# Performance work log

Measured on AMD Instinct MI355X. Metric: run time of the kernel, lower is better.

Reference implementation:

```python
import jax, jax.numpy as jnp
import numpy as np

D = 128      # input_dim (= out_channels = edge_dim)
H = 2        # n_head
N_ENT = 100000
B = 64       # number of queries / batches
R = 500      # number of relations
E = 400000   # number of original edges
NEG = 0.2    # GATv2 leaky_relu negative slope


def setup_inputs() -> dict:
    key = jax.random.key(0)
    ks = jax.random.split(key, 10)
    s = 1.0 / np.sqrt(D)
    queries = jax.random.normal(ks[0], (B, D), jnp.float32)
    entities = jax.random.normal(ks[1], (N_ENT, D), jnp.float32)
    edge_index = jax.random.randint(ks[2], (2, E), 0, N_ENT)
    relations = jax.random.normal(ks[3], (R, D), jnp.float32)
    relation_index = jax.random.randint(ks[4], (E,), 0, R)
    # guarantees batch.max()+1 == queries.shape[0] (module assert)
    batch = jnp.arange(N_ENT, dtype=jnp.int32) % B
    # GATv2Conv params: lin_l / lin_r (bias=True), lin_edge (bias=False), att, bias
    W_l = jax.random.normal(ks[5], (H * D, D), jnp.float32) * s
    b_l = jnp.zeros((H * D,), jnp.float32)
    W_r = jax.random.normal(ks[6], (H * D, D), jnp.float32) * s
    b_r = jnp.zeros((H * D,), jnp.float32)
    W_ea = jax.random.normal(ks[7], (H * D, D), jnp.float32) * s
    att = jax.random.normal(ks[8], (H, D), jnp.float32) * s
    bias = jnp.zeros((D,), jnp.float32)  # concat=False -> size out_channels
    # outer Injector.lin_edge: Linear(H*D, D, bias=True)
    W_le = jax.random.normal(ks[9], (D, H * D), jnp.float32) / np.sqrt(H * D)
    b_le = jnp.zeros((D,), jnp.float32)
    return dict(queries=queries, entities=entities, edge_index=edge_index,
                relations=relations, relation_index=relation_index, batch=batch,
                W_l=W_l, b_l=b_l, W_r=W_r, b_r=b_r, W_ea=W_ea, att=att,
                bias=bias, W_le=W_le, b_le=b_le)


def reference(queries, entities, edge_index, relations, relation_index, batch,
              W_l, b_l, W_r, b_r, W_ea, att, bias, W_le, b_le):
    n_ent = entities.shape[0]
    node = jnp.vstack([entities, queries])                        # [N+B, D]
    rel_feat = jnp.vstack([relations,
                           jnp.ones((1, relations.shape[1]), relations.dtype)])
    # added edges: query -> its entities
    src = jnp.concatenate([edge_index[0], batch.astype(edge_index.dtype) + n_ent])
    tgt = jnp.concatenate([edge_index[1],
                           jnp.arange(n_ent, dtype=edge_index.dtype)])
    rel_idx = jnp.concatenate([relation_index,
                               jnp.full((n_ent,), rel_feat.shape[0] - 1,
                                        relation_index.dtype)])
    edge_attr = rel_feat[rel_idx]                                  # [Etot, D]

    n_tot = node.shape[0]
    x_l = (node @ W_l.T + b_l).reshape(n_tot, H, D)                # source proj
    x_r = (node @ W_r.T + b_r).reshape(n_tot, H, D)                # target proj
    e = (edge_attr @ W_ea.T).reshape(-1, H, D)                     # [Etot, H, D]

    xj = x_l[src]                                                  # gather per edge
    z = jax.nn.leaky_relu(xj + x_r[tgt] + e, NEG)                  # [Etot, H, D]
    alpha = jnp.einsum('ehd,hd->eh', z, att)                       # [Etot, H]
    # segment softmax over target nodes
    amax = jax.ops.segment_max(alpha, tgt, num_segments=n_tot)
    alpha = jnp.exp(alpha - amax[tgt])
    denom = jax.ops.segment_sum(alpha, tgt, num_segments=n_tot)
    alpha = alpha / (denom[tgt] + 1e-16)

    msg = xj * alpha[..., None]                                    # [Etot, H, D]
    agg = jax.ops.segment_sum(msg, tgt, num_segments=n_tot)        # [Ntot, H, D]
    out = agg.mean(axis=1) + bias                                  # concat=False
    out_node = out[:n_ent]

    out_edge = jax.nn.relu(relations @ W_ea.T)                     # [R, H*D]
    out_edge = out_edge @ W_le.T + b_le                            # [R, D]
    return (out_node, out_edge)
```

## Files before the change

### kernel.cpp

```cpp
#include <hip/hip_runtime.h>
#include <math.h>

#define D 128
#define HD 256
#define N_ENT 100000
#define NBATCH 64
#define NTOT (N_ENT + NBATCH)
#define RCOUNT 500
#define E_BASE 400000
#define ETOT (E_BASE + N_ENT)
#define NEG 0.2f
#define SCAN_NB 391
#define CPAD (SCAN_NB * 256)

#define WCAST_NB 64
#define ZERO_NB SCAN_NB
#define REL_NB (RCOUNT + 1)
#define PREP_NB (WCAST_NB + ZERO_NB + REL_NB)

#define GEMM_NB ((NTOT + 63) / 64)
#define HIST_NB ((ETOT + 255) / 256)
#define EDGE_TPW 8
#define EDGE_NB (N_ENT / (4 * EDGE_TPW))

typedef __attribute__((ext_vector_type(8))) short bf16x8;
typedef __attribute__((ext_vector_type(8))) unsigned short u16x8;
typedef __attribute__((ext_vector_type(4))) float f32x4;
typedef __attribute__((ext_vector_type(2))) float f32x2;

static __device__ __forceinline__ unsigned cvt_pk_bf16(float lo, float hi) {
  unsigned r;
  asm("v_cvt_pk_bf16_f32 %0, %1, %2" : "=v"(r) : "v"(lo), "v"(hi));
  return r;
}
static __device__ __forceinline__ unsigned short f2bf_hw(float f) {
  unsigned r;
  asm("v_cvt_pk_bf16_f32 %0, %1, %1" : "=v"(r) : "v"(f));
  return (unsigned short)r;
}
static __device__ __forceinline__ f32x2 bfpair(unsigned u) {
  f32x2 r;
  r[0] = __builtin_bit_cast(float, u << 16);
  r[1] = __builtin_bit_cast(float, u & 0xffff0000u);
  return r;
}

static __device__ __forceinline__ float dpp_red16(float p) {
  int t;
  t = __builtin_amdgcn_update_dpp(0, __builtin_bit_cast(int, p), 0xB1, 0xF, 0xF, true);
  p += __builtin_bit_cast(float, t);
  t = __builtin_amdgcn_update_dpp(0, __builtin_bit_cast(int, p), 0x4E, 0xF, 0xF, true);
  p += __builtin_bit_cast(float, t);
  t = __builtin_amdgcn_update_dpp(0, __builtin_bit_cast(int, p), 0x141, 0xF, 0xF, true);
  p += __builtin_bit_cast(float, t);
  t = __builtin_amdgcn_update_dpp(0, __builtin_bit_cast(int, p), 0x140, 0xF, 0xF, true);
  p += __builtin_bit_cast(float, t);
  return p;
}

__global__ __launch_bounds__(256) void k_prep(
    const float* __restrict__ W_l, const float* __restrict__ W_r,
    unsigned short* __restrict__ Wbf,
    const float* __restrict__ relations, const float* __restrict__ W_ea,
    const float* __restrict__ W_le, const float* __restrict__ b_le,
    unsigned short* __restrict__ e_rel, float* __restrict__ out_edge,
    int* __restrict__ counts) {
  __shared__ float relu_p[HD];
  int bx = blockIdx.x;
  int tid = threadIdx.x;
  if (bx < WCAST_NB) {
    int e4 = (bx * 256 + tid) * 4;
    int v = e4 >> 7;
    int k = e4 & 127;
    const float* src = (v < HD) ? (W_l + (size_t)v * D + k) : (W_r + (size_t)(v - HD) * D + k);
    float4 a = *(const float4*)src;
    uint2 p;
    p.x = cvt_pk_bf16(a.x, a.y);
    p.y = cvt_pk_bf16(a.z, a.w);
    *(uint2*)(Wbf + (size_t)v * D + k) = p;
    return;
  }
  if (bx < WCAST_NB + ZERO_NB) {
    counts[(bx - WCAST_NB) * 256 + tid] = 0;
    return;
  }
  int r = bx - (WCAST_NB + ZERO_NB);
  int j = tid;
  const float* w = W_ea + (size_t)j * D;
  float acc = 0.f;
  if (r < RCOUNT) {
    const float* rel = relations + (size_t)r * D;
    for (int k = 0; k < D; k += 4) {
      float4 a = *(const float4*)(rel + k);
      float4 b = *(const float4*)(w + k);
      acc += a.x * b.x + a.y * b.y + a.z * b.z + a.w * b.w;
    }
  } else {
    for (int k = 0; k < D; k += 4) {
      float4 b = *(const float4*)(w + k);
      acc += b.x + b.y + b.z + b.w;
    }
  }
  e_rel[(size_t)r * HD + j] = f2bf_hw(acc);
  if (r < RCOUNT) {
    relu_p[j] = acc > 0.f ? acc : 0.f;
    __syncthreads();
    if (j < D) {
      const float* wl = W_le + (size_t)j * HD;
      float o = b_le[j];
      for (int k = 0; k < HD; k += 4) {
        float4 p4 = *(const float4*)(relu_p + k);
        float4 w4 = *(const float4*)(wl + k);
        o += p4.x * w4.x + p4.y * w4.y + p4.z * w4.z + p4.w * w4.w;
      }
      out_edge[(size_t)r * D + j] = o;
    }
  }
}

#define LDA 136

__global__ __launch_bounds__(256) void k_gemm_mfma(
    const float* __restrict__ entities, const float* __restrict__ queries,
    const unsigned short* __restrict__ Wbf,
    const float* __restrict__ b_l, const float* __restrict__ b_r,
    unsigned short* __restrict__ x_l, unsigned short* __restrict__ x_r,
    const int* __restrict__ edge_index, int* __restrict__ counts,
    int* __restrict__ rank) {
  __shared__ unsigned short As[64 * LDA];
  __shared__ unsigned short Cs[64 * LDA];
  int tid = threadIdx.x;
  if (blockIdx.x >= GEMM_NB) {
    int e = (blockIdx.x - GEMM_NB) * 256 + tid;
    if (e < ETOT) {
      int t = (e < E_BASE) ? edge_index[E_BASE + e] : (e - E_BASE);
      rank[e] = atomicAdd(counts + t, 1);
    }
    return;
  }
  int rb = blockIdx.x;

  {
    int rr = tid >> 2;
    int part = (tid & 3) * 32;
    int row = rb * 64 + rr;
    const float* sp;
    if (row < N_ENT) sp = entities + (size_t)row * D;
    else if (row < NTOT) sp = queries + (size_t)(row - N_ENT) * D;
    else sp = entities;
#pragma unroll
    for (int k = 0; k < 32; k += 8) {
      float4 a0 = *(const float4*)(sp + part + k);
      float4 a1 = *(const float4*)(sp + part + k + 4);
      uint4 p;
      p.x = cvt_pk_bf16(a0.x, a0.y);
      p.y = cvt_pk_bf16(a0.z, a0.w);
      p.z = cvt_pk_bf16(a1.x, a1.y);
      p.w = cvt_pk_bf16(a1.z, a1.w);
      *(uint4*)(&As[rr * LDA + part + k]) = p;
    }
  }
  __syncthreads();

  int w = tid >> 6, lane = tid & 63;
  int wr = w >> 1, wc = w & 1;
  int m = lane & 15, q8 = (lane >> 4) * 8;

  for (int ccv = 0; ccv < 4; ccv++) {
    bool isL = ccv < 2;
    const float* bv = isL ? b_l : b_r;
    unsigned short* xdst = isL ? x_l : x_r;
    int cbase = (ccv & 1) * 128;

    f32x4 acc[2][4];
#pragma unroll
    for (int i = 0; i < 2; i++)
#pragma unroll
      for (int j = 0; j < 4; j++) acc[i][j] = (f32x4){0.f, 0.f, 0.f, 0.f};

    const unsigned short* wbase = Wbf + (size_t)(ccv * 128 + wc * 64 + m) * D;
#pragma unroll
    for (int ks = 0; ks < 128; ks += 32) {
      bf16x8 af[2], bfr[4];
#pragma unroll
      for (int i = 0; i < 2; i++)
        af[i] = *(const bf16x8*)(&As[(wr * 32 + i * 16 + m) * LDA + ks + q8]);
#pragma unroll
      for (int j = 0; j < 4; j++)
        bfr[j] = *(const bf16x8*)(wbase + (size_t)j * 16 * D + ks + q8);
#pragma unroll
      for (int i = 0; i < 2; i++)
#pragma unroll
        for (int j = 0; j < 4; j++)
          acc[i][j] = __builtin_amdgcn_mfma_f32_16x16x32_bf16(af[i], bfr[j], acc[i][j], 0, 0, 0);
    }

    __syncthreads();
#pragma unroll
    for (int j = 0; j < 4; j++) {
      int col = wc * 64 + j * 16 + m;
      float bb = bv[cbase + col];
#pragma unroll
      for (int i = 0; i < 2; i++) {
        int row0 = wr * 32 + i * 16 + (lane >> 4) * 4;
#pragma unroll
        for (int r = 0; r < 4; r++)
          Cs[(row0 + r) * LDA + col] = f2bf_hw(acc[i][j][r] + bb);
      }
    }
    __syncthreads();
#pragma unroll
    for (int it = 0; it < 4; it++) {
      int g = it * 256 + tid;
      int row = g >> 4, c8 = (g & 15) * 8;
      int grow = rb * 64 + row;
      if (grow < NTOT) {
        u16x8 v = *(const u16x8*)(&Cs[row * LDA + c8]);
        *(u16x8*)(xdst + (size_t)grow * HD + cbase + c8) = v;
      }
    }
  }
}

__global__ __launch_bounds__(256) void k_scan_a(const int* __restrict__ counts, int* __restrict__ bsum) {
  __shared__ int sd[256];
  int tid = threadIdx.x;
  sd[tid] = counts[blockIdx.x * 256 + tid];
  __syncthreads();
  for (int off = 128; off > 0; off >>= 1) {
    if (tid < off) sd[tid] += sd[tid + off];
    __syncthreads();
  }
  if (tid == 0) bsum[blockIdx.x] = sd[0];
}

__global__ __launch_bounds__(256) void k_scan_b(
    const int* __restrict__ counts, const int* __restrict__ bsum,
    int* __restrict__ offsets) {
  __shared__ int s[256];
  int b = blockIdx.x, tid = threadIdx.x;
  int part = 0;
  if (tid < b) part += bsum[tid];
  if (tid + 256 < b) part += bsum[tid + 256];
  s[tid] = part;
  __syncthreads();
  for (int off = 128; off > 0; off >>= 1) {
    if (tid < off) s[tid] += s[tid + off];
    __syncthreads();
  }
  int pre_sum = s[0];
  __syncthreads();
  int v = counts[b * 256 + tid];
  s[tid] = v;
  __syncthreads();
  for (int off = 1; off < 256; off <<= 1) {
    int y = (tid >= off) ? s[tid - off] : 0;
    __syncthreads();
    s[tid] += y;
    __syncthreads();
  }
  int excl = pre_sum + s[tid] - v;
  int i = b * 256 + tid;
  if (i <= N_ENT) offsets[i] = excl;
}

__global__ void k_scatter(const int* __restrict__ edge_index, const int* __restrict__ relation_index,
                          const int* __restrict__ batch, const int* __restrict__ offsets,
                          const int* __restrict__ rank, unsigned* __restrict__ sorted) {
  int e = blockIdx.x * 256 + threadIdx.x;
  if (e >= ETOT) return;
  int s, t, r;
  if (e < E_BASE) {
    s = edge_index[e];
    t = edge_index[E_BASE + e];
    r = relation_index[e];
  } else {
    int i = e - E_BASE;
    s = N_ENT + batch[i];
    t = i;
    r = RCOUNT;
  }
  int pos = offsets[t] + rank[e];
  sorted[pos] = (unsigned)s | ((unsigned)r << 17);
}

static __device__ __forceinline__ float edge_accum(
    u16x8 xl8, u16x8 er8, const f32x2* __restrict__ xr2,
    const f32x2* __restrict__ at2, f32x2* __restrict__ x2) {
  uint4 xu = __builtin_bit_cast(uint4, xl8);
  uint4 eu = __builtin_bit_cast(uint4, er8);
  unsigned xw[4] = {xu.x, xu.y, xu.z, xu.w};
  unsigned ew[4] = {eu.x, eu.y, eu.z, eu.w};
  f32x2 p2 = (f32x2){0.f, 0.f};
#pragma unroll
  for (int i = 0; i < 4; ++i) {
    f32x2 x = bfpair(xw[i]);
    x2[i] = x;
    f32x2 z = (x + xr2[i]) + bfpair(ew[i]);
    f32x2 zn = z * NEG;
    z[0] = fmaxf(z[0], zn[0]);
    z[1] = fmaxf(z[1], zn[1]);
    p2 += z * at2[i];
  }
  return p2[0] + p2[1];
}

__global__ __launch_bounds__(256) void k_edge(
    const unsigned short* __restrict__ x_l, const unsigned short* __restrict__ x_r,
    const unsigned short* __restrict__ e_rel, const int* __restrict__ offsets,
    const unsigned* __restrict__ sorted, const float* __restrict__ att,
    const float* __restrict__ bias, float* __restrict__ out) {
  int wv = threadIdx.x >> 6;
  int lane = threadIdx.x & 63;
  int half = lane >> 5;
  int sl = lane & 31;
  int elem = sl * 8;
  int t0 = (blockIdx.x * 4 + wv) * EDGE_TPW;

  const char* xlb = (const char*)x_l + elem * 2;
  const char* erb = (const char*)e_rel + elem * 2;

  f32x2 at2[4];
  {
    float4 a0 = *(const float4*)(att + elem);
    float4 a1 = *(const float4*)(att + elem + 4);
    at2[0] = (f32x2){a0.x, a0.y};
    at2[1] = (f32x2){a0.z, a0.w};
    at2[2] = (f32x2){a1.x, a1.y};
    at2[3] = (f32x2){a1.z, a1.w};
  }
  int eb[EDGE_TPW + 1];
  {
    int4 o0 = *(const int4*)(offsets + t0);
    int4 o1 = *(const int4*)(offsets + t0 + 4);
    eb[0] = o0.x; eb[1] = o0.y; eb[2] = o0.z; eb[3] = o0.w;
    eb[4] = o1.x; eb[5] = o1.y; eb[6] = o1.z; eb[7] = o1.w;
    eb[8] = offsets[t0 + 8];
  }

  u16x8 xr8 = __builtin_nontemporal_load((const u16x8*)(x_r + (size_t)t0 * HD + elem));

#pragma unroll
  for (int ti = 0; ti < EDGE_TPW; ++ti) {
    f32x2 xr2[4];
    {
      uint4 u = __builtin_bit_cast(uint4, xr8);
      xr2[0] = bfpair(u.x); xr2[1] = bfpair(u.y);
      xr2[2] = bfpair(u.z); xr2[3] = bfpair(u.w);
    }
    xr8 = __builtin_nontemporal_load((const u16x8*)(x_r + (size_t)(t0 + ti + 1) * HD + elem));

    int e0 = eb[ti], e1 = eb[ti + 1];
    f32x2 acc2[4];
    acc2[0] = acc2[1] = acc2[2] = acc2[3] = (f32x2){0.f, 0.f};
    float denom = 0.f;
    int e = e0;
    for (; e + 4 <= e1; e += 4) {
      unsigned srA = sorted[e + half];
      unsigned srB = sorted[e + 2 + half];
      u16x8 xlA = *(const u16x8*)(xlb + ((size_t)(srA & 0x1FFFFu) << 9));
      u16x8 erA = *(const u16x8*)(erb + ((size_t)(srA >> 17) << 9));
      u16x8 xlB = *(const u16x8*)(xlb + ((size_t)(srB & 0x1FFFFu) << 9));
      u16x8 erB = *(const u16x8*)(erb + ((size_t)(srB >> 17) << 9));
      f32x2 xa2[4], xb2[4];
      float pa = edge_accum(xlA, erA, xr2, at2, xa2);
      float pb = edge_accum(xlB, erB, xr2, at2, xb2);
      pa = dpp_red16(pa);
      pb = dpp_red16(pb);
      float wa = __expf(pa);
      float wb = __expf(pb);
      denom += wa + wb;
#pragma unroll
      for (int i = 0; i < 4; ++i) {
        acc2[i] += xa2[i] * wa;
        acc2[i] += xb2[i] * wb;
      }
    }
    for (; e < e1; e += 2) {
      int ee = e + half;
      bool valid = ee < e1;
      unsigned sr = sorted[valid ? ee : e0];
      u16x8 xl8 = *(const u16x8*)(xlb + ((size_t)(sr & 0x1FFFFu) << 9));
      u16x8 er8 = *(const u16x8*)(erb + ((size_t)(sr >> 17) << 9));
      f32x2 x2[4];
      float p = edge_accum(xl8, er8, xr2, at2, x2);
      p = dpp_red16(p);
      float wgt = valid ? __expf(p) : 0.f;
      denom += wgt;
#pragma unroll
      for (int i = 0; i < 4; ++i) acc2[i] += x2[i] * wgt;
    }
    denom += __shfl_xor(denom, 32, 64);
#pragma unroll
    for (int i = 0; i < 4; ++i) {
      acc2[i][0] += __shfl_xor(acc2[i][0], 32, 64);
      acc2[i][1] += __shfl_xor(acc2[i][1], 32, 64);
    }
    float inv = 0.5f / (denom + 1e-16f);
    float o[8];
#pragma unroll
    for (int i = 0; i < 4; ++i) {
      o[2 * i] = acc2[i][0] * inv;
      o[2 * i + 1] = acc2[i][1] * inv;
    }
#pragma unroll
    for (int i = 0; i < 8; ++i) o[i] += __shfl_xor(o[i], 16, 64);
    if (lane < 16) {
      int t = t0 + ti;
      int d = sl * 8;
      float4 b0 = *(const float4*)(bias + d);
      float4 b1 = *(const float4*)(bias + d + 4);
      f32x4 s0 = (f32x4){o[0] + b0.x, o[1] + b0.y, o[2] + b0.z, o[3] + b0.w};
      f32x4 s1 = (f32x4){o[4] + b1.x, o[5] + b1.y, o[6] + b1.z, o[7] + b1.w};
      __builtin_nontemporal_store(s0, (f32x4*)(out + (size_t)t * D + d));
      __builtin_nontemporal_store(s1, (f32x4*)(out + (size_t)t * D + d + 4));
    }
  }
}

extern "C" void kernel_launch(void* const* d_in, const int* in_sizes, int n_in,
                              void* d_out, int out_size, void* d_ws, size_t ws_size,
                              hipStream_t stream) {
  const float* queries = (const float*)d_in[0];
  const float* entities = (const float*)d_in[1];
  const int* edge_index = (const int*)d_in[2];
  const float* relations = (const float*)d_in[3];
  const int* relation_index = (const int*)d_in[4];
  const int* batch = (const int*)d_in[5];
  const float* W_l = (const float*)d_in[6];
  const float* b_l = (const float*)d_in[7];
  const float* W_r = (const float*)d_in[8];
  const float* b_r = (const float*)d_in[9];
  const float* W_ea = (const float*)d_in[10];
  const float* att = (const float*)d_in[11];
  const float* bias = (const float*)d_in[12];
  const float* W_le = (const float*)d_in[13];
  const float* b_le = (const float*)d_in[14];

  float* out_node = (float*)d_out;
  float* out_edge = out_node + (size_t)N_ENT * D;

  char* base = (char*)d_ws;
  size_t off = 0;
  auto take = [&](size_t nbytes) -> void* {
    void* p = base + off;
    off += (nbytes + 255) & ~(size_t)255;
    return p;
  };
  unsigned short* x_l = (unsigned short*)take((size_t)NTOT * HD * sizeof(unsigned short));
  unsigned short* x_r = (unsigned short*)take((size_t)NTOT * HD * sizeof(unsigned short));
  unsigned short* e_rel = (unsigned short*)take((size_t)(RCOUNT + 1) * HD * sizeof(unsigned short));
  unsigned short* Wbf = (unsigned short*)take((size_t)512 * D * sizeof(unsigned short));
  int* counts = (int*)take((size_t)CPAD * sizeof(int));
  int* offsets = (int*)take((size_t)(N_ENT + 1) * sizeof(int));
  int* rank = (int*)take((size_t)ETOT * sizeof(int));
  int* bsum = (int*)take(512 * sizeof(int));
  unsigned* sorted = (unsigned*)take((size_t)ETOT * sizeof(unsigned));

  k_prep<<<dim3(PREP_NB), dim3(256), 0, stream>>>(W_l, W_r, Wbf, relations, W_ea, W_le, b_le,
                                                  e_rel, out_edge, counts);
  k_gemm_mfma<<<dim3(GEMM_NB + HIST_NB), dim3(256), 0, stream>>>(entities, queries, Wbf, b_l, b_r,
                                                                 x_l, x_r, edge_index, counts, rank);
  k_scan_a<<<dim3(SCAN_NB), dim3(256), 0, stream>>>(counts, bsum);
  k_scan_b<<<dim3(SCAN_NB), dim3(256), 0, stream>>>(counts, bsum, offsets);
  k_scatter<<<dim3(HIST_NB), dim3(256), 0, stream>>>(edge_index, relation_index, batch, offsets, rank, sorted);
  k_edge<<<dim3(EDGE_NB), dim3(256), 0, stream>>>(x_l, x_r, e_rel, offsets, sorted, att, bias, out_node);
}
```

Measured before the change: 286.2 us.

## Precompute packed edge keys in histogram pass, memset counts, shrink edge tiles

The histogram pass now packs target and rank, plus source and relation, into two arrays, so the scatter kernel reads two words per edge instead of re-reading edge_index, relation_index and batch. Zeroing counts moves from extra k_prep blocks to hipMemsetAsync. The GEMM uses nontemporal loads for entities and nontemporal stores for x_l/x_r. The edge kernel handles 4 targets per wave instead of 8, doubling the grid. Together these trade an extra write of packed keys and an added memset call for less scatter-side gather work and more parallelism in the edge kernel.

```diff
diff --git a/kernel.cpp b/kernel.cpp
--- a/kernel.cpp
+++ b/kernel.cpp
@@ -14,14 +14,12 @@
 #define CPAD (SCAN_NB * 256)
 
 #define WCAST_NB 64
-#define ZERO_NB SCAN_NB
 #define REL_NB (RCOUNT + 1)
-#define PREP_NB (WCAST_NB + ZERO_NB + REL_NB)
+#define PREP_NB (WCAST_NB + REL_NB)
 
 #define GEMM_NB ((NTOT + 63) / 64)
 #define HIST_NB ((ETOT + 255) / 256)
-#define EDGE_TPW 8
-#define EDGE_NB (N_ENT / (4 * EDGE_TPW))
+#define EDGE_NB 6250
 
 typedef __attribute__((ext_vector_type(8))) short bf16x8;
 typedef __attribute__((ext_vector_type(8))) unsigned short u16x8;
@@ -63,8 +61,7 @@
     unsigned short* __restrict__ Wbf,
     const float* __restrict__ relations, const float* __restrict__ W_ea,
     const float* __restrict__ W_le, const float* __restrict__ b_le,
-    unsigned short* __restrict__ e_rel, float* __restrict__ out_edge,
-    int* __restrict__ counts) {
+    unsigned short* __restrict__ e_rel, float* __restrict__ out_edge) {
   __shared__ float relu_p[HD];
   int bx = blockIdx.x;
   int tid = threadIdx.x;
@@ -80,11 +77,7 @@
     *(uint2*)(Wbf + (size_t)v * D + k) = p;
     return;
   }
-  if (bx < WCAST_NB + ZERO_NB) {
-    counts[(bx - WCAST_NB) * 256 + tid] = 0;
-    return;
-  }
-  int r = bx - (WCAST_NB + ZERO_NB);
+  int r = bx - WCAST_NB;
   int j = tid;
   const float* w = W_ea + (size_t)j * D;
   float acc = 0.f;
@@ -125,16 +118,29 @@
     const unsigned short* __restrict__ Wbf,
     const float* __restrict__ b_l, const float* __restrict__ b_r,
     unsigned short* __restrict__ x_l, unsigned short* __restrict__ x_r,
-    const int* __restrict__ edge_index, int* __restrict__ counts,
-    int* __restrict__ rank) {
+    const int* __restrict__ edge_index, const int* __restrict__ relation_index,
+    const int* __restrict__ batch, int* __restrict__ counts,
+    unsigned* __restrict__ tr, unsigned* __restrict__ key) {
   __shared__ unsigned short As[64 * LDA];
   __shared__ unsigned short Cs[64 * LDA];
   int tid = threadIdx.x;
   if (blockIdx.x >= GEMM_NB) {
     int e = (blockIdx.x - GEMM_NB) * 256 + tid;
     if (e < ETOT) {
-      int t = (e < E_BASE) ? edge_index[E_BASE + e] : (e - E_BASE);
-      rank[e] = atomicAdd(counts + t, 1);
+      int s, t, r;
+      if (e < E_BASE) {
+        s = edge_index[e];
+        t = edge_index[E_BASE + e];
+        r = relation_index[e];
+      } else {
+        int i = e - E_BASE;
+        s = N_ENT + batch[i];
+        t = i;
+        r = RCOUNT;
+      }
+      int rk = atomicAdd(counts + t, 1);
+      tr[e] = (unsigned)t | ((unsigned)rk << 17);
+      key[e] = (unsigned)s | ((unsigned)r << 17);
     }
     return;
   }
@@ -150,13 +156,13 @@
     else sp = entities;
 #pragma unroll
     for (int k = 0; k < 32; k += 8) {
-      float4 a0 = *(const float4*)(sp + part + k);
-      float4 a1 = *(const float4*)(sp + part + k + 4);
+      f32x4 a0 = __builtin_nontemporal_load((const f32x4*)(sp + part + k));
+      f32x4 a1 = __builtin_nontemporal_load((const f32x4*)(sp + part + k + 4));
       uint4 p;
-      p.x = cvt_pk_bf16(a0.x, a0.y);
-      p.y = cvt_pk_bf16(a0.z, a0.w);
-      p.z = cvt_pk_bf16(a1.x, a1.y);
-      p.w = cvt_pk_bf16(a1.z, a1.w);
+      p.x = cvt_pk_bf16(a0[0], a0[1]);
+      p.y = cvt_pk_bf16(a0[2], a0[3]);
+      p.z = cvt_pk_bf16(a1[0], a1[1]);
+      p.w = cvt_pk_bf16(a1[2], a1[3]);
       *(uint4*)(&As[rr * LDA + part + k]) = p;
     }
   }
@@ -216,7 +222,7 @@
       int grow = rb * 64 + row;
       if (grow < NTOT) {
         u16x8 v = *(const u16x8*)(&Cs[row * LDA + c8]);
-        *(u16x8*)(xdst + (size_t)grow * HD + cbase + c8) = v;
+        __builtin_nontemporal_store(v, (u16x8*)(xdst + (size_t)grow * HD + cbase + c8));
       }
     }
   }
@@ -264,24 +270,12 @@
   if (i <= N_ENT) offsets[i] = excl;
 }
 
-__global__ void k_scatter(const int* __restrict__ edge_index, const int* __restrict__ relation_index,
-                          const int* __restrict__ batch, const int* __restrict__ offsets,
-                          const int* __restrict__ rank, unsigned* __restrict__ sorted) {
+__global__ void k_scatter(const unsigned* __restrict__ tr, const unsigned* __restrict__ key,
+                          const int* __restrict__ offsets, unsigned* __restrict__ sorted) {
   int e = blockIdx.x * 256 + threadIdx.x;
   if (e >= ETOT) return;
-  int s, t, r;
-  if (e < E_BASE) {
-    s = edge_index[e];
-    t = edge_index[E_BASE + e];
-    r = relation_index[e];
-  } else {
-    int i = e - E_BASE;
-    s = N_ENT + batch[i];
-    t = i;
-    r = RCOUNT;
-  }
-  int pos = offsets[t] + rank[e];
-  sorted[pos] = (unsigned)s | ((unsigned)r << 17);
+  unsigned a = tr[e];
+  sorted[offsets[a & 0x1FFFFu] + (a >> 17)] = key[e];
 }
 
 static __device__ __forceinline__ float edge_accum(
@@ -315,7 +309,7 @@
   int half = lane >> 5;
   int sl = lane & 31;
   int elem = sl * 8;
-  int t0 = (blockIdx.x * 4 + wv) * EDGE_TPW;
+  int t0 = (blockIdx.x * 4 + wv) * 4;
 
   const char* xlb = (const char*)x_l + elem * 2;
   const char* erb = (const char*)e_rel + elem * 2;
@@ -329,19 +323,15 @@
     at2[2] = (f32x2){a1.x, a1.y};
     at2[3] = (f32x2){a1.z, a1.w};
   }
-  int eb[EDGE_TPW + 1];
-  {
-    int4 o0 = *(const int4*)(offsets + t0);
-    int4 o1 = *(const int4*)(offsets + t0 + 4);
-    eb[0] = o0.x; eb[1] = o0.y; eb[2] = o0.z; eb[3] = o0.w;
-    eb[4] = o1.x; eb[5] = o1.y; eb[6] = o1.z; eb[7] = o1.w;
-    eb[8] = offsets[t0 + 8];
-  }
+  int4 ofs = *(const int4*)(offsets + t0);
+  int eb[5];
+  eb[0] = ofs.x; eb[1] = ofs.y; eb[2] = ofs.z; eb[3] = ofs.w;
+  eb[4] = offsets[t0 + 4];
 
   u16x8 xr8 = __builtin_nontemporal_load((const u16x8*)(x_r + (size_t)t0 * HD + elem));
 
 #pragma unroll
-  for (int ti = 0; ti < EDGE_TPW; ++ti) {
+  for (int ti = 0; ti < 4; ++ti) {
     f32x2 xr2[4];
     {
       uint4 u = __builtin_bit_cast(uint4, xr8);
@@ -453,16 +443,19 @@
   unsigned short* Wbf = (unsigned short*)take((size_t)512 * D * sizeof(unsigned short));
   int* counts = (int*)take((size_t)CPAD * sizeof(int));
   int* offsets = (int*)take((size_t)(N_ENT + 1) * sizeof(int));
-  int* rank = (int*)take((size_t)ETOT * sizeof(int));
+  unsigned* tr = (unsigned*)take((size_t)ETOT * sizeof(unsigned));
+  unsigned* key = (unsigned*)take((size_t)ETOT * sizeof(unsigned));
   int* bsum = (int*)take(512 * sizeof(int));
   unsigned* sorted = (unsigned*)take((size_t)ETOT * sizeof(unsigned));
 
+  hipMemsetAsync(counts, 0, (size_t)CPAD * sizeof(int), stream);
   k_prep<<<dim3(PREP_NB), dim3(256), 0, stream>>>(W_l, W_r, Wbf, relations, W_ea, W_le, b_le,
-                                                  e_rel, out_edge, counts);
+                                                  e_rel, out_edge);
   k_gemm_mfma<<<dim3(GEMM_NB + HIST_NB), dim3(256), 0, stream>>>(entities, queries, Wbf, b_l, b_r,
-                                                                 x_l, x_r, edge_index, counts, rank);
+                                                                 x_l, x_r, edge_index, relation_index,
+                                                                 batch, counts, tr, key);
   k_scan_a<<<dim3(SCAN_NB), dim3(256), 0, stream>>>(counts, bsum);
   k_scan_b<<<dim3(SCAN_NB), dim3(256), 0, stream>>>(counts, bsum, offsets);
-  k_scatter<<<dim3(HIST_NB), dim3(256), 0, stream>>>(edge_index, relation_index, batch, offsets, rank, sorted);
+  k_scatter<<<dim3(HIST_NB), dim3(256), 0, stream>>>(tr, key, offsets, sorted);
   k_edge<<<dim3(EDGE_NB), dim3(256), 0, stream>>>(x_l, x_r, e_rel, offsets, sorted, att, bias, out_node);
 }
```

Result: slower. 326.1 us (+13.9%).
